# Kernel tuning notes

Measured on AMD Instinct MI355X. Metric: run time of the kernel, lower is better.

The kernel has to match this reference:

```python
import jax, jax.numpy as jnp
import numpy as np

M = 131072  # KV length
DK = 256    # key dim
DV = 256    # value dim


def setup_inputs() -> dict:
    key = jax.random.key(0)
    k1, k2, k3 = jax.random.split(key, 3)
    q = jax.random.normal(k1, (DK,), dtype=jnp.float32)
    K = jax.random.normal(k2, (M, DK), dtype=jnp.float32)
    V = jax.random.normal(k3, (M, DV), dtype=jnp.float32)
    return {"q": q, "K": K, "V": V}


def reference(q, K, V):
    # logits[m] = sum_k K[m,k] * q[k]
    logits = jnp.einsum('mk,k->m', K, q)
    # stable softmax over the m axis
    weights = jax.nn.softmax(logits, axis=-1)
    # y[v] = sum_m weights[m] * V[m,v]
    return jnp.einsum('m,mv->v', weights, V)
```

## Files before the change

kernel.cpp:

```cpp
#include <hip/hip_runtime.h>
#include <math.h>

#define DKD 256
#define DVD 256

constexpr int RPB   = 128;
constexpr int TPB   = 256;
constexpr int WAVES = TPB / 64;

__global__ __launch_bounds__(TPB, 4) void attn_pass1(
    const float* __restrict__ q,
    const float* __restrict__ K,
    const float* __restrict__ V,
    float* __restrict__ m_arr,
    float* __restrict__ l_arr,
    float* __restrict__ acc_arr,
    int M)
{
    __shared__ float  q_lds[DKD];
    __shared__ float  part[2][RPB];
    __shared__ float  e_lds[RPB];
    __shared__ float  red[RPB];
    __shared__ float4 s_acc[WAVES][64];
    __shared__ float  s_l;

    const int t    = threadIdx.x;
    const int lane = t & 63;
    const int wave = t >> 6;
    const int b    = blockIdx.x;
    const int row_begin = b * RPB;

    q_lds[t] = q[t];
    __syncthreads();

    const float4* __restrict__ K4  = (const float4*)K;
    const float4* __restrict__ V4  = (const float4*)V;
    const float4* q4l = (const float4*)q_lds;

    const int rowA  = t & (RPB - 1);
    const int halfA = t >> 7;
    const int growc = min(row_begin + rowA, M - 1);

    float4 d = make_float4(0.f, 0.f, 0.f, 0.f);
    const size_t kbase = (size_t)growc * (DKD / 4) + halfA * (DKD / 8);
    #pragma unroll 8
    for (int j = 0; j < DKD / 8; ++j) {
        const float4 kv = K4[kbase + j];
        const float4 qv = q4l[halfA * (DKD / 8) + j];
        d.x += kv.x * qv.x; d.y += kv.y * qv.y;
        d.z += kv.z * qv.z; d.w += kv.w * qv.w;
    }
    part[halfA][rowA] = d.x + d.y + d.z + d.w;
    __syncthreads();

    float logit = 0.f;
    if (t < RPB) {
        logit = part[0][t] + part[1][t];
        if (row_begin + t >= M) logit = -INFINITY;
        red[t] = logit;
    }
    __syncthreads();
    #pragma unroll
    for (int s = RPB / 2; s > 0; s >>= 1) {
        if (t < s) red[t] = fmaxf(red[t], red[t + s]);
        __syncthreads();
    }
    float bm = red[0];
    if (bm == -INFINITY) bm = 0.f;
    __syncthreads();
    if (t < RPB) {
        float e = __expf(logit - bm);
        if (row_begin + t >= M) e = 0.f;
        e_lds[t] = e;
        red[t] = e;
    }
    __syncthreads();
    #pragma unroll
    for (int s = RPB / 2; s > 0; s >>= 1) {
        if (t < s) red[t] += red[t + s];
        __syncthreads();
    }
    if (t == 0) s_l = red[0];

    float4 acc = make_float4(0.f, 0.f, 0.f, 0.f);
    const int rw = wave * (RPB / WAVES);
    for (int it = 0; it < (RPB / WAVES) / 8; ++it) {
        const int r0 = rw + it * 8;
        #pragma unroll
        for (int u = 0; u < 8; ++u) {
            const int rl = r0 + u;
            const int gv = min(row_begin + rl, M - 1);
            const float  e  = e_lds[rl];
            const float4 vv = V4[(size_t)gv * (DVD / 4) + lane];
            acc.x += e * vv.x; acc.y += e * vv.y;
            acc.z += e * vv.z; acc.w += e * vv.w;
        }
    }
    s_acc[wave][lane] = acc;
    __syncthreads();

    float yv = 0.f;
    const float* saf = (const float*)&s_acc[0][0];
    #pragma unroll
    for (int w = 0; w < WAVES; ++w) yv += saf[w * DVD + t];
    acc_arr[(size_t)b * DVD + t] = yv;
    if (t == 0) { m_arr[b] = bm; l_arr[b] = s_l; }
}

__global__ __launch_bounds__(256) void attn_pass2(
    const float* __restrict__ m_arr,
    const float* __restrict__ l_arr,
    const float* __restrict__ acc_arr,
    float* __restrict__ out,
    int nb)
{
    __shared__ float red[256];
    const int t = threadIdx.x;

    float lm = -INFINITY;
    for (int b = t; b < nb; b += 256) lm = fmaxf(lm, m_arr[b]);
    red[t] = lm; __syncthreads();
    for (int s = 128; s > 0; s >>= 1) {
        if (t < s) red[t] = fmaxf(red[t], red[t + s]);
        __syncthreads();
    }
    const float Mg = red[0];
    __syncthreads();

    float ll = 0.0f;
    for (int b = t; b < nb; b += 256) ll += l_arr[b] * __expf(m_arr[b] - Mg);
    red[t] = ll; __syncthreads();
    for (int s = 128; s > 0; s >>= 1) {
        if (t < s) red[t] += red[t + s];
        __syncthreads();
    }
    const float invL = 1.0f / red[0];
    __syncthreads();

    const int j = blockIdx.x;
    float part = 0.0f;
    for (int b = t; b < nb; b += 256)
        part += __expf(m_arr[b] - Mg) * acc_arr[(size_t)b * DVD + j];

    red[t] = part; __syncthreads();
    for (int s = 128; s > 0; s >>= 1) {
        if (t < s) red[t] += red[t + s];
        __syncthreads();
    }
    if (t == 0) out[j] = red[0] * invL;
}

extern "C" void kernel_launch(void* const* d_in, const int* in_sizes, int n_in,
                              void* d_out, int out_size, void* d_ws, size_t ws_size,
                              hipStream_t stream) {
    const float* q = (const float*)d_in[0];
    const float* K = (const float*)d_in[1];
    const float* V = (const float*)d_in[2];
    float* out = (float*)d_out;

    const int M  = in_sizes[1] / DKD;
    const int nb = (M + RPB - 1) / RPB;

    float* ws      = (float*)d_ws;
    float* m_arr   = ws;
    float* l_arr   = ws + nb;
    float* acc_arr = ws + 2 * nb;

    attn_pass1<<<nb, TPB, 0, stream>>>(q, K, V, m_arr, l_arr, acc_arr, M);
    attn_pass2<<<DVD, 256, 0, stream>>>(m_arr, l_arr, acc_arr, out, nb);
}
```

Before: 283.3 us.

## Stage K and V tiles into LDS with double-buffered async global-to-LDS loads

Each block now handles 256 rows instead of 128. K and V are streamed through two 32-row LDS buffers using global_load_lds async copies, so the next tile loads while the current one is computed. The V staging for the second phase starts during the last K tile. The dot product moves to an 8-lane-per-row layout with shuffle reductions. In exchange, LDS use per block grows a lot and the grid halves, which lowers occupancy and parallelism. Correctness also depends on the async LDS writes being complete at the barriers.

```diff
diff --git a/kernel.cpp b/kernel.cpp
--- a/kernel.cpp
+++ b/kernel.cpp
@@ -4,11 +4,33 @@
 #define DKD 256
 #define DVD 256
 
-constexpr int RPB   = 128;
-constexpr int TPB   = 256;
-constexpr int WAVES = TPB / 64;
+constexpr int RPB    = 256;
+constexpr int TILE_R = 32;
+constexpr int NTILES = RPB / TILE_R;
+constexpr int TPB    = 256;
+constexpr int WAVES  = 4;
 
-__global__ __launch_bounds__(TPB, 4) void attn_pass1(
+__device__ __forceinline__ void async_row16(const float* g, float* l) {
+    __builtin_amdgcn_global_load_lds(
+        (const __attribute__((address_space(1))) void*)g,
+        (__attribute__((address_space(3))) void*)l,
+        16, 0, 0);
+}
+
+__device__ __forceinline__ void stage_tile(const float* __restrict__ src,
+                                           int g_row0, int M,
+                                           float* lbuf, int wave, int lane) {
+    #pragma unroll
+    for (int i = 0; i < TILE_R / WAVES; ++i) {
+        const int lrow = wave * (TILE_R / WAVES) + i;
+        int grow = g_row0 + lrow;
+        grow = grow < M ? grow : M - 1;
+        async_row16(src + (size_t)grow * DKD + lane * 4,
+                    lbuf + lrow * DKD);
+    }
+}
+
+__global__ __launch_bounds__(TPB, 2) void attn_pass1(
     const float* __restrict__ q,
     const float* __restrict__ K,
     const float* __restrict__ V,
@@ -17,10 +39,10 @@
     float* __restrict__ acc_arr,
     int M)
 {
+    __shared__ float  buf[2][TILE_R * DKD];
     __shared__ float  q_lds[DKD];
-    __shared__ float  part[2][RPB];
     __shared__ float  e_lds[RPB];
-    __shared__ float  red[RPB];
+    __shared__ float  red[TPB];
     __shared__ float4 s_acc[WAVES][64];
     __shared__ float  s_l;
 
@@ -31,74 +53,79 @@
     const int row_begin = b * RPB;
 
     q_lds[t] = q[t];
+    stage_tile(K, row_begin, M, buf[0], wave, lane);
+
+    const int seg  = lane & 7;
+    const int rsub = lane >> 3;
+    for (int kt = 0; kt < NTILES; ++kt) {
+        __syncthreads();
+        if (kt + 1 < NTILES)
+            stage_tile(K, row_begin + (kt + 1) * TILE_R, M, buf[(kt + 1) & 1], wave, lane);
+        else
+            stage_tile(V, row_begin, M, buf[NTILES & 1], wave, lane);
+
+        const int rloc = wave * 8 + rsub;
+        const float4* krow = (const float4*)(buf[kt & 1] + rloc * DKD);
+        const float4* q4   = (const float4*)q_lds;
+        float4 d = make_float4(0.f, 0.f, 0.f, 0.f);
+        #pragma unroll
+        for (int j = 0; j < 8; ++j) {
+            const float4 kv = krow[seg + 8 * j];
+            const float4 qv = q4[seg + 8 * j];
+            d.x += kv.x * qv.x; d.y += kv.y * qv.y;
+            d.z += kv.z * qv.z; d.w += kv.w * qv.w;
+        }
+        float s = d.x + d.y + d.z + d.w;
+        s += __shfl_xor(s, 1);
+        s += __shfl_xor(s, 2);
+        s += __shfl_xor(s, 4);
+        if (seg == 0) e_lds[kt * TILE_R + rloc] = s;
+    }
+
     __syncthreads();
-
-    const float4* __restrict__ K4  = (const float4*)K;
-    const float4* __restrict__ V4  = (const float4*)V;
-    const float4* q4l = (const float4*)q_lds;
-
-    const int rowA  = t & (RPB - 1);
-    const int halfA = t >> 7;
-    const int growc = min(row_begin + rowA, M - 1);
-
-    float4 d = make_float4(0.f, 0.f, 0.f, 0.f);
-    const size_t kbase = (size_t)growc * (DKD / 4) + halfA * (DKD / 8);
-    #pragma unroll 8
-    for (int j = 0; j < DKD / 8; ++j) {
-        const float4 kv = K4[kbase + j];
-        const float4 qv = q4l[halfA * (DKD / 8) + j];
-        d.x += kv.x * qv.x; d.y += kv.y * qv.y;
-        d.z += kv.z * qv.z; d.w += kv.w * qv.w;
-    }
-    part[halfA][rowA] = d.x + d.y + d.z + d.w;
-    __syncthreads();
-
-    float logit = 0.f;
-    if (t < RPB) {
-        logit = part[0][t] + part[1][t];
-        if (row_begin + t >= M) logit = -INFINITY;
-        red[t] = logit;
-    }
+    float logit = e_lds[t];
+    if (row_begin + t >= M) logit = -INFINITY;
+    red[t] = logit;
     __syncthreads();
     #pragma unroll
-    for (int s = RPB / 2; s > 0; s >>= 1) {
+    for (int s = 128; s > 0; s >>= 1) {
         if (t < s) red[t] = fmaxf(red[t], red[t + s]);
         __syncthreads();
     }
     float bm = red[0];
     if (bm == -INFINITY) bm = 0.f;
     __syncthreads();
-    if (t < RPB) {
-        float e = __expf(logit - bm);
-        if (row_begin + t >= M) e = 0.f;
-        e_lds[t] = e;
-        red[t] = e;
-    }
+    const float e = (row_begin + t < M) ? __expf(logit - bm) : 0.f;
+    e_lds[t] = e;
+    red[t]   = e;
     __syncthreads();
     #pragma unroll
-    for (int s = RPB / 2; s > 0; s >>= 1) {
+    for (int s = 128; s > 0; s >>= 1) {
         if (t < s) red[t] += red[t + s];
         __syncthreads();
     }
     if (t == 0) s_l = red[0];
 
     float4 acc = make_float4(0.f, 0.f, 0.f, 0.f);
-    const int rw = wave * (RPB / WAVES);
-    for (int it = 0; it < (RPB / WAVES) / 8; ++it) {
-        const int r0 = rw + it * 8;
+    for (int vt = 0; vt < NTILES; ++vt) {
+        __syncthreads();
+        if (vt + 1 < NTILES)
+            stage_tile(V, row_begin + (vt + 1) * TILE_R, M,
+                       buf[(NTILES + vt + 1) & 1], wave, lane);
+
+        const float* vb = buf[(NTILES + vt) & 1];
         #pragma unroll
         for (int u = 0; u < 8; ++u) {
-            const int rl = r0 + u;
-            const int gv = min(row_begin + rl, M - 1);
-            const float  e  = e_lds[rl];
-            const float4 vv = V4[(size_t)gv * (DVD / 4) + lane];
-            acc.x += e * vv.x; acc.y += e * vv.y;
-            acc.z += e * vv.z; acc.w += e * vv.w;
+            const int rloc = wave * 8 + u;
+            const float  ew = e_lds[vt * TILE_R + rloc];
+            const float4 vv = ((const float4*)vb)[rloc * 64 + lane];
+            acc.x += ew * vv.x; acc.y += ew * vv.y;
+            acc.z += ew * vv.z; acc.w += ew * vv.w;
         }
     }
+
     s_acc[wave][lane] = acc;
     __syncthreads();
-
     float yv = 0.f;
     const float* saf = (const float*)&s_acc[0][0];
     #pragma unroll
```

Result: no change. 280.6 us (-0.9%).
